# Kernel tuning notes

Measured on AMD Instinct MI355X. Metric: run time of the kernel, lower is better.

Reference implementation:

```python
import jax, jax.numpy as jnp
import numpy as np

N_NODES = 100000
N_EDGES = 3200000
N_GRAPHS = 1000


def setup_inputs() -> dict:
    key = jax.random.key(0)
    ks = jax.random.split(key, 12)
    inp = {
        "x": jax.random.normal(ks[0], (N_NODES, 4), dtype=jnp.float32),
        "W1": jax.random.normal(ks[1], (4, 64), dtype=jnp.float32) * 0.5,
        "b1": jax.random.normal(ks[2], (64,), dtype=jnp.float32) * 0.1,
        "W2": jax.random.normal(ks[3], (64, 32), dtype=jnp.float32) * 0.125,
        "b2": jax.random.normal(ks[4], (32,), dtype=jnp.float32) * 0.1,
        "W3": jax.random.normal(ks[5], (32, 16), dtype=jnp.float32) * 0.17,
        "b3": jax.random.normal(ks[6], (16,), dtype=jnp.float32) * 0.1,
        "Wl": jax.random.normal(ks[7], (16, 1), dtype=jnp.float32) * 0.25,
        "bl": jax.random.normal(ks[8], (1,), dtype=jnp.float32) * 0.1,
        "edge_index": jax.random.randint(ks[9], (2, N_EDGES), 0, N_NODES, dtype=jnp.int32),
        "batch": jnp.sort(jax.random.randint(ks[10], (N_NODES,), 0, N_GRAPHS, dtype=jnp.int32)),
    }
    return inp


def _gcn_conv(h, W, b, src, dst, norm, num_nodes):
    # PyG GCNConv: transform, then normalized scatter-add over edges (incl. self-loops)
    h = h @ W                                    # [N, out]
    msg = h[src] * norm[:, None]                 # [E+N, out]
    out = jax.ops.segment_sum(msg, dst, num_segments=num_nodes)
    return out + b


def reference(x, W1, b1, W2, b2, W3, b3, Wl, bl, edge_index, batch):
    num_nodes = x.shape[0]
    num_graphs = N_GRAPHS
    loop = jnp.arange(num_nodes, dtype=edge_index.dtype)
    src = jnp.concatenate([edge_index[0], loop])  # edges + self-loops
    dst = jnp.concatenate([edge_index[1], loop])
    # symmetric degree normalization: deg over destination incl. self-loops
    deg = jax.ops.segment_sum(jnp.ones_like(dst, dtype=x.dtype), dst, num_segments=num_nodes)
    dinv = jnp.where(deg > 0, jax.lax.rsqrt(deg), 0.0)
    norm = dinv[src] * dinv[dst]                 # [E+N]

    h = jax.nn.relu(_gcn_conv(x, W1, b1, src, dst, norm, num_nodes))
    h = jax.nn.relu(_gcn_conv(h, W2, b2, src, dst, norm, num_nodes))
    h = _gcn_conv(h, W3, b3, src, dst, norm, num_nodes)

    # global_mean_pool
    sums = jax.ops.segment_sum(h, batch, num_segments=num_graphs)        # [G,16]
    cnts = jax.ops.segment_sum(jnp.ones((num_nodes,), x.dtype), batch, num_segments=num_graphs)
    pooled = sums / jnp.maximum(cnts, 1.0)[:, None]

    return jax.nn.relu(pooled @ Wl + bl)          # [G,1]
```

## Files before the change

kernel.cpp:

```cpp
#include <hip/hip_runtime.h>
#include <hip/hip_fp16.h>

#define N_NODES 100000
#define N_EDGES 3200000
#define N_GRAPHS 1000
#define NB 1024
#define NPB 98
#define CAP 3584
#define EPB 8192


__global__ void k_zero(int* __restrict__ bcnt) {
    int i = blockIdx.x * blockDim.x + threadIdx.x;
    if (i < NB) bcnt[i] = 0;
}

__global__ __launch_bounds__(256) void k_bucket(
    const int* __restrict__ src, const int* __restrict__ dst,
    int* __restrict__ bcnt, unsigned* __restrict__ pay) {
    __shared__ int cnt[NB];
    __shared__ int off[NB];
    __shared__ int scanbuf[256];
    __shared__ unsigned rec[EPB];

    int tid = threadIdx.x;
    int e0 = blockIdx.x * EPB;
    for (int i = tid; i < NB; i += 256) cnt[i] = 0;
    __syncthreads();

#pragma unroll
    for (int k = 0; k < EPB / 256; ++k) {
        int e = e0 + k * 256 + tid;
        if (e < N_EDGES) atomicAdd(&cnt[(unsigned)dst[e] / NPB], 1);
    }
    __syncthreads();

    int base = tid * 4;
    int c0 = cnt[base], c1 = cnt[base + 1], c2 = cnt[base + 2], c3 = cnt[base + 3];
    int part = c0 + c1 + c2 + c3;
    scanbuf[tid] = part;
    __syncthreads();
    for (int o = 1; o < 256; o <<= 1) {
        int v = (tid >= o) ? scanbuf[tid - o] : 0;
        __syncthreads();
        scanbuf[tid] += v;
        __syncthreads();
    }
    int ex = scanbuf[tid] - part;
    off[base]     = ex;
    off[base + 1] = ex + c0;
    off[base + 2] = ex + c0 + c1;
    off[base + 3] = ex + c0 + c1 + c2;
    __syncthreads();

#pragma unroll
    for (int k = 0; k < EPB / 256; ++k) {
        int e = e0 + k * 256 + tid;
        if (e < N_EDGES) {
            unsigned s = (unsigned)src[e];
            unsigned d = (unsigned)dst[e];
            unsigned b = d / NPB;
            unsigned ld = d - b * NPB;
            int p = atomicAdd(&off[b], 1);
            rec[p] = s | (ld << 17);
        }
    }
    __syncthreads();

    for (int b = tid; b < NB; b += 256) {
        int c = cnt[b];
        if (c == 0) continue;
        int ls = off[b] - c;
        int gb = atomicAdd(&bcnt[b], c);
        unsigned* dstp = pay + (size_t)b * CAP;
        for (int k = 0; k < c; ++k) {
            int gp = gb + k;
            if (gp < CAP) dstp[gp] = rec[ls + k];
        }
    }
}

__global__ __launch_bounds__(256) void k_sort(
    unsigned* __restrict__ pay, const int* __restrict__ bcnt,
    const float* __restrict__ x, float* __restrict__ dinv,
    float* __restrict__ xp, int* __restrict__ row, int* __restrict__ dgar) {
    __shared__ unsigned rec[CAP], rec2[CAP];
    __shared__ int hl[NPB], st[NPB], ofl[NPB];
    int tid = threadIdx.x;
    int b = blockIdx.x;
    int cnt = bcnt[b]; if (cnt > CAP) cnt = CAP;
    unsigned* P = pay + (size_t)b * CAP;

    if (tid < NPB) hl[tid] = 0;
    __syncthreads();

    for (int i = tid; i < cnt; i += 256) {
        unsigned w = P[i];
        rec[i] = w;
        atomicAdd(&hl[w >> 17], 1);
    }
    __syncthreads();

    if (tid == 0) {
        int run = 0;
        for (int l = 0; l < NPB; ++l) { st[l] = run; run += hl[l]; }
    }
    __syncthreads();
    if (tid < NPB) ofl[tid] = st[tid];

    if (tid < NPB) {
        int n = b * NPB + tid;
        if (n < N_NODES) {
            row[n]  = b * CAP + st[tid];
            dgar[n] = hl[tid];
            float di = rsqrtf((float)(hl[tid] + 1));
            dinv[n] = di;
            float4 v = reinterpret_cast<const float4*>(x)[n];
            v.x *= di; v.y *= di; v.z *= di; v.w *= di;
            reinterpret_cast<float4*>(xp)[n] = v;
        }
    }
    __syncthreads();

    for (int i = tid; i < cnt; i += 256) {
        unsigned w = rec[i];
        int p = atomicAdd(&ofl[w >> 17], 1);
        rec2[p] = w;
    }
    __syncthreads();

    for (int i = tid; i < cnt; i += 256) P[i] = rec2[i];
}

__global__ __launch_bounds__(256) void k_g1(
    const float* __restrict__ xp, const unsigned* __restrict__ pay,
    const int* __restrict__ row, const int* __restrict__ dgar,
    float* __restrict__ agg1) {
    int tid = threadIdx.x;
    int lane = tid & 3;
    int n = blockIdx.x * 64 + (tid >> 2);
    if (n >= N_NODES) return;
    int r = row[n], d = dgar[n];
    const unsigned* P = pay + r;
    float acc = 0.0f;
#pragma unroll 4
    for (int j = 0; j < d; ++j) {
        int sn = P[j] & 0x1FFFF;
        acc += xp[sn * 4 + lane];
    }
    agg1[(size_t)n * 4 + lane] = acc;
}

__global__ __launch_bounds__(256) void k_dense1(
    const float* __restrict__ agg1, const float* __restrict__ xp,
    const float* __restrict__ dinv,
    const float* __restrict__ W1, const float* __restrict__ b1,
    const float* __restrict__ W2, __half* __restrict__ t2ph) {
    __shared__ float sW1[256], sb1[64], sW2[2048];
    int tid = threadIdx.x;
    sW1[tid] = W1[tid];
    if (tid < 64) sb1[tid] = b1[tid];
    for (int i = tid; i < 2048; i += 256) sW2[i] = W2[i];
    __syncthreads();

    int n = blockIdx.x * 256 + tid;
    if (n >= N_NODES) return;
    float di = dinv[n];
    float4 ag = reinterpret_cast<const float4*>(agg1)[n];
    float4 sv = reinterpret_cast<const float4*>(xp)[n];
    float a[4] = {(ag.x + sv.x) * di, (ag.y + sv.y) * di,
                  (ag.z + sv.z) * di, (ag.w + sv.w) * di};
    float t[32];
#pragma unroll
    for (int k = 0; k < 32; ++k) t[k] = 0.0f;
    for (int j = 0; j < 64; ++j) {
        float h = sb1[j];
#pragma unroll
        for (int i = 0; i < 4; ++i) h += a[i] * sW1[i * 64 + j];
        h = fmaxf(h, 0.0f);
#pragma unroll
        for (int k = 0; k < 32; ++k) t[k] += h * sW2[j * 32 + k];
    }
    __half2* o = reinterpret_cast<__half2*>(t2ph + (size_t)n * 32);
#pragma unroll
    for (int q = 0; q < 16; ++q)
        o[q] = __floats2half2_rn(t[2*q] * di, t[2*q+1] * di);
}

__global__ __launch_bounds__(256) void k_g2(
    const __half* __restrict__ t2ph, const unsigned* __restrict__ pay,
    const int* __restrict__ row, const int* __restrict__ dgar,
    float* __restrict__ agg2) {
    int tid = threadIdx.x;
    int lane = tid & 3;
    int n = blockIdx.x * 64 + (tid >> 2);
    if (n >= N_NODES) return;
    int r = row[n], d = dgar[n];
    const unsigned* P = pay + r;
    float a0 = 0, a1 = 0, a2 = 0, a3 = 0, a4 = 0, a5 = 0, a6 = 0, a7 = 0;
#pragma unroll 4
    for (int j = 0; j < d; ++j) {
        int sn = P[j] & 0x1FFFF;
        union { uint4 u; __half2 h[4]; } U;
        U.u = *reinterpret_cast<const uint4*>(t2ph + (size_t)sn * 32 + lane * 8);
        float2 f0 = __half22float2(U.h[0]);
        float2 f1 = __half22float2(U.h[1]);
        float2 f2 = __half22float2(U.h[2]);
        float2 f3 = __half22float2(U.h[3]);
        a0 += f0.x; a1 += f0.y; a2 += f1.x; a3 += f1.y;
        a4 += f2.x; a5 += f2.y; a6 += f3.x; a7 += f3.y;
    }
    float4* o = reinterpret_cast<float4*>(agg2 + (size_t)n * 32 + lane * 8);
    o[0] = make_float4(a0, a1, a2, a3);
    o[1] = make_float4(a4, a5, a6, a7);
}

__global__ __launch_bounds__(256) void k_dense2(
    const float* __restrict__ agg2, const __half* __restrict__ t2ph,
    const float* __restrict__ dinv,
    const float* __restrict__ b2, const float* __restrict__ W3,
    __half* __restrict__ t3ph) {
    __shared__ float sb2[32], sW3[512];
    int tid = threadIdx.x;
    if (tid < 32) sb2[tid] = b2[tid];
    for (int i = tid; i < 512; i += 256) sW3[i] = W3[i];
    __syncthreads();

    int n = blockIdx.x * 256 + tid;
    if (n >= N_NODES) return;
    float di = dinv[n];
    const float2* ag = reinterpret_cast<const float2*>(agg2 + (size_t)n * 32);
    const __half2* sp = reinterpret_cast<const __half2*>(t2ph + (size_t)n * 32);
    float h[32];
#pragma unroll
    for (int q = 0; q < 16; ++q) {
        float2 a = ag[q];
        float2 sv = __half22float2(sp[q]);
        h[2*q]   = fmaxf((a.x + sv.x) * di + sb2[2*q],   0.0f);
        h[2*q+1] = fmaxf((a.y + sv.y) * di + sb2[2*q+1], 0.0f);
    }
    float t[16];
#pragma unroll
    for (int k = 0; k < 16; ++k) t[k] = 0.0f;
    for (int j = 0; j < 32; ++j) {
#pragma unroll
        for (int k = 0; k < 16; ++k) t[k] += h[j] * sW3[j * 16 + k];
    }
    __half2* o = reinterpret_cast<__half2*>(t3ph + (size_t)n * 16);
#pragma unroll
    for (int q = 0; q < 8; ++q)
        o[q] = __floats2half2_rn(t[2*q] * di, t[2*q+1] * di);
}

__global__ __launch_bounds__(256) void k_g3(
    const __half* __restrict__ t3ph, const unsigned* __restrict__ pay,
    const int* __restrict__ row, const int* __restrict__ dgar,
    const float* __restrict__ dinv, const float* __restrict__ b3,
    const float* __restrict__ Wl, float* __restrict__ sval) {
    int tid = threadIdx.x;
    int lane = tid & 3;
    int n = blockIdx.x * 64 + (tid >> 2);
    if (n >= N_NODES) return;
    int r = row[n], d = dgar[n];
    const unsigned* P = pay + r;
    float a0 = 0, a1 = 0, a2 = 0, a3 = 0;
#pragma unroll 4
    for (int j = 0; j < d; ++j) {
        int sn = P[j] & 0x1FFFF;
        union { uint2 u; __half2 h[2]; } U;
        U.u = *reinterpret_cast<const uint2*>(t3ph + (size_t)sn * 16 + lane * 4);
        float2 f0 = __half22float2(U.h[0]);
        float2 f1 = __half22float2(U.h[1]);
        a0 += f0.x; a1 += f0.y; a2 += f1.x; a3 += f1.y;
    }
    union { uint2 u; __half2 h[2]; } S;
    S.u = *reinterpret_cast<const uint2*>(t3ph + (size_t)n * 16 + lane * 4);
    float2 s0 = __half22float2(S.h[0]);
    float2 s1 = __half22float2(S.h[1]);
    float di = dinv[n];
    float p = ((a0 + s0.x) * di + b3[lane * 4 + 0]) * Wl[lane * 4 + 0]
            + ((a1 + s0.y) * di + b3[lane * 4 + 1]) * Wl[lane * 4 + 1]
            + ((a2 + s1.x) * di + b3[lane * 4 + 2]) * Wl[lane * 4 + 2]
            + ((a3 + s1.y) * di + b3[lane * 4 + 3]) * Wl[lane * 4 + 3];
    p += __shfl_xor(p, 1);
    p += __shfl_xor(p, 2);
    if (lane == 0) sval[n] = p;
}

__global__ __launch_bounds__(64) void k_poolg(
    const float* __restrict__ sval, const int* __restrict__ batch,
    const float* __restrict__ bl, float* __restrict__ out) {
    int g = blockIdx.x;
    int lo = 0, hi = N_NODES;
    while (lo < hi) { int m = (lo + hi) >> 1; if (batch[m] < g) lo = m + 1; else hi = m; }
    int s0 = lo;
    hi = N_NODES;
    while (lo < hi) { int m = (lo + hi) >> 1; if (batch[m] < g + 1) lo = m + 1; else hi = m; }
    int s1 = lo;
    float s = 0.0f;
    for (int i = s0 + threadIdx.x; i < s1; i += 64) s += sval[i];
#pragma unroll
    for (int o = 32; o > 0; o >>= 1) s += __shfl_down(s, o);
    if (threadIdx.x == 0) {
        float c = fmaxf((float)(s1 - s0), 1.0f);
        out[g] = fmaxf(s / c + bl[0], 0.0f);
    }
}

extern "C" void kernel_launch(void* const* d_in, const int* in_sizes, int n_in,
                              void* d_out, int out_size, void* d_ws, size_t ws_size,
                              hipStream_t stream) {
    const float* x  = (const float*)d_in[0];
    const float* W1 = (const float*)d_in[1];
    const float* b1 = (const float*)d_in[2];
    const float* W2 = (const float*)d_in[3];
    const float* b2 = (const float*)d_in[4];
    const float* W3 = (const float*)d_in[5];
    const float* b3 = (const float*)d_in[6];
    const float* Wl = (const float*)d_in[7];
    const float* bl = (const float*)d_in[8];
    const int*   ei = (const int*)d_in[9];
    const int* batch = (const int*)d_in[10];
    const int* src = ei;
    const int* dst = ei + N_EDGES;
    float* out = (float*)d_out;

    const size_t N = N_NODES;
    char* ws = (char*)d_ws;
    float*    dinv = (float*)   (ws);
    float*    xp   = (float*)   (ws + 4 * (N));
    __half*   t2ph = (__half*)  (ws + 4 * (5 * N));
    __half*   t3ph = (__half*)  (ws + 4 * (21 * N));
    float*    agg1 = (float*)   (ws + 4 * (29 * N));
    float*    agg2 = (float*)   (ws + 4 * (33 * N));
    float*    sval = (float*)   (ws + 4 * (65 * N));
    int*      row  = (int*)     (ws + 4 * (81 * N));
    int*      dgar = (int*)     (ws + 4 * (82 * N));
    int*      bcnt = (int*)     (ws + 4 * (83 * N));
    unsigned* pay  = (unsigned*)(ws + 4 * (83 * N + NB));

    const int B = 256;
    const int gN = (N_NODES + B - 1) / B;
    const int gB = (N_EDGES + EPB - 1) / EPB;
    const int gG = (N_NODES + 63) / 64;

    k_zero  <<<(NB + B - 1) / B, B, 0, stream>>>(bcnt);
    k_bucket<<<gB, B, 0, stream>>>(src, dst, bcnt, pay);
    k_sort  <<<NB, B, 0, stream>>>(pay, bcnt, x, dinv, xp, row, dgar);
    k_g1    <<<gG, B, 0, stream>>>(xp, pay, row, dgar, agg1);
    k_dense1<<<gN, B, 0, stream>>>(agg1, xp, dinv, W1, b1, W2, t2ph);
    k_g2    <<<gG, B, 0, stream>>>(t2ph, pay, row, dgar, agg2);
    k_dense2<<<gN, B, 0, stream>>>(agg2, t2ph, dinv, b2, W3, t3ph);
    k_g3    <<<gG, B, 0, stream>>>(t3ph, pay, row, dgar, dinv, b3, Wl, sval);
    k_poolg <<<N_GRAPHS, 64, 0, stream>>>(sval, batch, bl, out);
}
```

Measured before the change: 272.3 us.

## Split layer-2 feature table into two 16-channel halves gathered in separate passes

The 32-channel fp16 layer-2 table is split into two 16-channel tables (32 bytes per node each). The gather kernel runs twice, once per half, so each pass's random-access working set is half as large (3.2MB vs 6.4MB) and fits better in L2/MALL. The cost is reading the edge payload list twice and one extra kernel launch.

```diff
diff --git a/kernel.cpp b/kernel.cpp
--- a/kernel.cpp
+++ b/kernel.cpp
@@ -155,7 +155,8 @@
     const float* __restrict__ agg1, const float* __restrict__ xp,
     const float* __restrict__ dinv,
     const float* __restrict__ W1, const float* __restrict__ b1,
-    const float* __restrict__ W2, __half* __restrict__ t2ph) {
+    const float* __restrict__ W2, __half* __restrict__ t2A,
+    __half* __restrict__ t2B) {
     __shared__ float sW1[256], sb1[64], sW2[2048];
     int tid = threadIdx.x;
     sW1[tid] = W1[tid];
@@ -181,42 +182,42 @@
 #pragma unroll
         for (int k = 0; k < 32; ++k) t[k] += h * sW2[j * 32 + k];
     }
-    __half2* o = reinterpret_cast<__half2*>(t2ph + (size_t)n * 32);
-#pragma unroll
-    for (int q = 0; q < 16; ++q)
-        o[q] = __floats2half2_rn(t[2*q] * di, t[2*q+1] * di);
-}
-
-__global__ __launch_bounds__(256) void k_g2(
-    const __half* __restrict__ t2ph, const unsigned* __restrict__ pay,
+    __half2* oA = reinterpret_cast<__half2*>(t2A + (size_t)n * 16);
+    __half2* oB = reinterpret_cast<__half2*>(t2B + (size_t)n * 16);
+#pragma unroll
+    for (int q = 0; q < 8; ++q) {
+        oA[q] = __floats2half2_rn(t[2*q]      * di, t[2*q+1]      * di);
+        oB[q] = __floats2half2_rn(t[16 + 2*q] * di, t[16 + 2*q+1] * di);
+    }
+}
+
+__global__ __launch_bounds__(256) void k_g2h(
+    const __half* __restrict__ tbl, const unsigned* __restrict__ pay,
     const int* __restrict__ row, const int* __restrict__ dgar,
-    float* __restrict__ agg2) {
+    float* __restrict__ aggOut) {
     int tid = threadIdx.x;
     int lane = tid & 3;
     int n = blockIdx.x * 64 + (tid >> 2);
     if (n >= N_NODES) return;
     int r = row[n], d = dgar[n];
     const unsigned* P = pay + r;
-    float a0 = 0, a1 = 0, a2 = 0, a3 = 0, a4 = 0, a5 = 0, a6 = 0, a7 = 0;
+    float a0 = 0, a1 = 0, a2 = 0, a3 = 0;
 #pragma unroll 4
     for (int j = 0; j < d; ++j) {
         int sn = P[j] & 0x1FFFF;
-        union { uint4 u; __half2 h[4]; } U;
-        U.u = *reinterpret_cast<const uint4*>(t2ph + (size_t)sn * 32 + lane * 8);
+        union { uint2 u; __half2 h[2]; } U;
+        U.u = *reinterpret_cast<const uint2*>(tbl + (size_t)sn * 16 + lane * 4);
         float2 f0 = __half22float2(U.h[0]);
         float2 f1 = __half22float2(U.h[1]);
-        float2 f2 = __half22float2(U.h[2]);
-        float2 f3 = __half22float2(U.h[3]);
         a0 += f0.x; a1 += f0.y; a2 += f1.x; a3 += f1.y;
-        a4 += f2.x; a5 += f2.y; a6 += f3.x; a7 += f3.y;
-    }
-    float4* o = reinterpret_cast<float4*>(agg2 + (size_t)n * 32 + lane * 8);
-    o[0] = make_float4(a0, a1, a2, a3);
-    o[1] = make_float4(a4, a5, a6, a7);
+    }
+    *reinterpret_cast<float4*>(aggOut + (size_t)n * 16 + lane * 4) =
+        make_float4(a0, a1, a2, a3);
 }
 
 __global__ __launch_bounds__(256) void k_dense2(
-    const float* __restrict__ agg2, const __half* __restrict__ t2ph,
+    const float* __restrict__ aggA, const float* __restrict__ aggB,
+    const __half* __restrict__ t2A, const __half* __restrict__ t2B,
     const float* __restrict__ dinv,
     const float* __restrict__ b2, const float* __restrict__ W3,
     __half* __restrict__ t3ph) {
@@ -229,15 +230,24 @@
     int n = blockIdx.x * 256 + tid;
     if (n >= N_NODES) return;
     float di = dinv[n];
-    const float2* ag = reinterpret_cast<const float2*>(agg2 + (size_t)n * 32);
-    const __half2* sp = reinterpret_cast<const __half2*>(t2ph + (size_t)n * 32);
+    const float2* agA = reinterpret_cast<const float2*>(aggA + (size_t)n * 16);
+    const float2* agB = reinterpret_cast<const float2*>(aggB + (size_t)n * 16);
+    const __half2* spA = reinterpret_cast<const __half2*>(t2A + (size_t)n * 16);
+    const __half2* spB = reinterpret_cast<const __half2*>(t2B + (size_t)n * 16);
     float h[32];
 #pragma unroll
-    for (int q = 0; q < 16; ++q) {
-        float2 a = ag[q];
-        float2 sv = __half22float2(sp[q]);
+    for (int q = 0; q < 8; ++q) {
+        float2 a = agA[q];
+        float2 sv = __half22float2(spA[q]);
         h[2*q]   = fmaxf((a.x + sv.x) * di + sb2[2*q],   0.0f);
         h[2*q+1] = fmaxf((a.y + sv.y) * di + sb2[2*q+1], 0.0f);
+    }
+#pragma unroll
+    for (int q = 0; q < 8; ++q) {
+        float2 a = agB[q];
+        float2 sv = __half22float2(spB[q]);
+        h[16+2*q]   = fmaxf((a.x + sv.x) * di + sb2[16+2*q],   0.0f);
+        h[16+2*q+1] = fmaxf((a.y + sv.y) * di + sb2[16+2*q+1], 0.0f);
     }
     float t[16];
 #pragma unroll
@@ -329,10 +339,12 @@
     char* ws = (char*)d_ws;
     float*    dinv = (float*)   (ws);
     float*    xp   = (float*)   (ws + 4 * (N));
-    __half*   t2ph = (__half*)  (ws + 4 * (5 * N));
+    __half*   t2A  = (__half*)  (ws + 4 * (5 * N));
+    __half*   t2B  = (__half*)  (ws + 4 * (13 * N));
     __half*   t3ph = (__half*)  (ws + 4 * (21 * N));
     float*    agg1 = (float*)   (ws + 4 * (29 * N));
-    float*    agg2 = (float*)   (ws + 4 * (33 * N));
+    float*    aggA = (float*)   (ws + 4 * (33 * N));
+    float*    aggB = (float*)   (ws + 4 * (49 * N));
     float*    sval = (float*)   (ws + 4 * (65 * N));
     int*      row  = (int*)     (ws + 4 * (81 * N));
     int*      dgar = (int*)     (ws + 4 * (82 * N));
@@ -348,9 +360,10 @@
     k_bucket<<<gB, B, 0, stream>>>(src, dst, bcnt, pay);
     k_sort  <<<NB, B, 0, stream>>>(pay, bcnt, x, dinv, xp, row, dgar);
     k_g1    <<<gG, B, 0, stream>>>(xp, pay, row, dgar, agg1);
-    k_dense1<<<gN, B, 0, stream>>>(agg1, xp, dinv, W1, b1, W2, t2ph);
-    k_g2    <<<gG, B, 0, stream>>>(t2ph, pay, row, dgar, agg2);
-    k_dense2<<<gN, B, 0, stream>>>(agg2, t2ph, dinv, b2, W3, t3ph);
+    k_dense1<<<gN, B, 0, stream>>>(agg1, xp, dinv, W1, b1, W2, t2A, t2B);
+    k_g2h   <<<gG, B, 0, stream>>>(t2A, pay, row, dgar, aggA);
+    k_g2h   <<<gG, B, 0, stream>>>(t2B, pay, row, dgar, aggB);
+    k_dense2<<<gN, B, 0, stream>>>(aggA, aggB, t2A, t2B, dinv, b2, W3, t3ph);
     k_g3    <<<gG, B, 0, stream>>>(t3ph, pay, row, dgar, dinv, b3, Wl, sval);
     k_poolg <<<N_GRAPHS, 64, 0, stream>>>(sval, batch, bl, out);
 }
```

Result: slower. 284.2 us (+4.4%).

## Cache edge records in registers, halve bucket block size, parallelize sort scan

Applied to the files above, without the earlier changes.

The bucketing kernel now loads each edge's src/dst once, packs the record and bucket id into registers, and reuses them for the scatter pass instead of re-reading global memory. Edges per block are halved, which doubles the number of blocks and the number of global bucket-count atomics and flushes. In the sort kernel, the serial single-thread prefix sum over 98 local node counts is replaced by a parallel Hillis-Steele scan over 128 entries. The register arrays raise register pressure, and the flush loop still copies each bucket serially.

```diff
diff --git a/kernel.cpp b/kernel.cpp
--- a/kernel.cpp
+++ b/kernel.cpp
@@ -7,7 +7,8 @@
 #define NB 1024
 #define NPB 98
 #define CAP 3584
-#define EPB 8192
+#define EPB 4096
+#define EPT 16
 
 
 __global__ void k_zero(int* __restrict__ bcnt) {
@@ -28,41 +29,47 @@
     for (int i = tid; i < NB; i += 256) cnt[i] = 0;
     __syncthreads();
 
-#pragma unroll
-    for (int k = 0; k < EPB / 256; ++k) {
-        int e = e0 + k * 256 + tid;
-        if (e < N_EDGES) atomicAdd(&cnt[(unsigned)dst[e] / NPB], 1);
-    }
-    __syncthreads();
-
-    int base = tid * 4;
-    int c0 = cnt[base], c1 = cnt[base + 1], c2 = cnt[base + 2], c3 = cnt[base + 3];
-    int part = c0 + c1 + c2 + c3;
-    scanbuf[tid] = part;
-    __syncthreads();
-    for (int o = 1; o < 256; o <<= 1) {
-        int v = (tid >= o) ? scanbuf[tid - o] : 0;
-        __syncthreads();
-        scanbuf[tid] += v;
-        __syncthreads();
-    }
-    int ex = scanbuf[tid] - part;
-    off[base]     = ex;
-    off[base + 1] = ex + c0;
-    off[base + 2] = ex + c0 + c1;
-    off[base + 3] = ex + c0 + c1 + c2;
-    __syncthreads();
-
-#pragma unroll
-    for (int k = 0; k < EPB / 256; ++k) {
+    unsigned wreg[EPT], breg[EPT];
+#pragma unroll
+    for (int k = 0; k < EPT; ++k) {
         int e = e0 + k * 256 + tid;
         if (e < N_EDGES) {
             unsigned s = (unsigned)src[e];
             unsigned d = (unsigned)dst[e];
             unsigned b = d / NPB;
             unsigned ld = d - b * NPB;
-            int p = atomicAdd(&off[b], 1);
-            rec[p] = s | (ld << 17);
+            wreg[k] = s | (ld << 17);
+            breg[k] = b;
+            atomicAdd(&cnt[b], 1);
+        } else {
+            breg[k] = 0xFFFFFFFFu;
+        }
+    }
+    __syncthreads();
+
+    int base = tid * 4;
+    int c0 = cnt[base], c1 = cnt[base + 1], c2 = cnt[base + 2], c3 = cnt[base + 3];
+    int part = c0 + c1 + c2 + c3;
+    scanbuf[tid] = part;
+    __syncthreads();
+    for (int o = 1; o < 256; o <<= 1) {
+        int v = (tid >= o) ? scanbuf[tid - o] : 0;
+        __syncthreads();
+        scanbuf[tid] += v;
+        __syncthreads();
+    }
+    int ex = scanbuf[tid] - part;
+    off[base]     = ex;
+    off[base + 1] = ex + c0;
+    off[base + 2] = ex + c0 + c1;
+    off[base + 3] = ex + c0 + c1 + c2;
+    __syncthreads();
+
+#pragma unroll
+    for (int k = 0; k < EPT; ++k) {
+        if (breg[k] != 0xFFFFFFFFu) {
+            int p = atomicAdd(&off[breg[k]], 1);
+            rec[p] = wreg[k];
         }
     }
     __syncthreads();
@@ -85,7 +92,7 @@
     const float* __restrict__ x, float* __restrict__ dinv,
     float* __restrict__ xp, int* __restrict__ row, int* __restrict__ dgar) {
     __shared__ unsigned rec[CAP], rec2[CAP];
-    __shared__ int hl[NPB], st[NPB], ofl[NPB];
+    __shared__ int hl[NPB], st[NPB], ofl[NPB], sc[128];
     int tid = threadIdx.x;
     int b = blockIdx.x;
     int cnt = bcnt[b]; if (cnt > CAP) cnt = CAP;
@@ -101,12 +108,21 @@
     }
     __syncthreads();
 
-    if (tid == 0) {
-        int run = 0;
-        for (int l = 0; l < NPB; ++l) { st[l] = run; run += hl[l]; }
-    }
-    __syncthreads();
-    if (tid < NPB) ofl[tid] = st[tid];
+    if (tid < 128) sc[tid] = (tid < NPB) ? hl[tid] : 0;
+    __syncthreads();
+    for (int o = 1; o < 128; o <<= 1) {
+        int v = 0;
+        if (tid < 128 && tid >= o) v = sc[tid - o];
+        __syncthreads();
+        if (tid < 128) sc[tid] += v;
+        __syncthreads();
+    }
+    if (tid < NPB) {
+        int s = sc[tid] - hl[tid];
+        st[tid] = s;
+        ofl[tid] = s;
+    }
+    __syncthreads();
 
     if (tid < NPB) {
         int n = b * NPB + tid;
```

Result: slower. 282.5 us (+3.8%).
